# Kernel tuning notes

Hardware: AMD Instinct MI355X
Metric: run time of the kernel (lower is better)

Reference implementation:

```python
import jax, jax.numpy as jnp
import numpy as np

B, T, D, E, H = 4, 1024, 1024, 8, 2048


def setup_inputs() -> dict:
    key = jax.random.key(0)
    ks = jax.random.split(key, 5)
    # Kaiming-uniform-ish init scales (exact values irrelevant for correctness baseline)
    bound_bank = 1.0 / np.sqrt(D)
    bound_down = 1.0 / np.sqrt(H)
    return {
        "x": jax.random.normal(ks[0], (B, T, D), dtype=jnp.float32),
        "gate_w": jax.random.uniform(ks[1], (E, D), jnp.float32, -bound_bank, bound_bank),
        "gate_bank": jax.random.uniform(ks[2], (E, D, H), jnp.float32, -bound_bank, bound_bank),
        "up_bank": jax.random.uniform(ks[3], (E, D, H), jnp.float32, -bound_bank, bound_bank),
        "down_bank": jax.random.uniform(ks[4], (E, H, D), jnp.float32, -bound_down, bound_down),
    }


def reference(x, gate_w, gate_bank, up_bank, down_bank):
    # Router logits: [B,T,E] (nn.Linear with weight [E,D], no bias)
    logits = jnp.einsum('btd,ed->bte', x, gate_w)
    selected = jnp.argmax(logits, axis=-1)          # [B,T] int
    # Dense all-expert SwiGLU
    u = jnp.einsum('btd,edh->bteh', x, up_bank)     # [B,T,E,H]
    a = jnp.einsum('btd,edh->bteh', x, gate_bank)   # [B,T,E,H]
    h = jax.nn.silu(a) * u                          # [B,T,E,H]
    y = jnp.einsum('bteh,ehd->bted', h, down_bank)  # [B,T,E,D]
    # Gather argmax-selected expert output per token
    idx = selected[:, :, None, None]                # [B,T,1,1]
    out = jnp.take_along_axis(y, idx, axis=2)[:, :, 0, :]  # [B,T,D]
    return out
```

## Files before the change

### kernel.cpp

```cpp
#include <hip/hip_runtime.h>
#include <hip/hip_bf16.h>

#define NTOK 4096
#define DDIM 1024
#define HDIM 2048
#define NEXP 8

typedef __attribute__((ext_vector_type(4))) float f32x4;
typedef __attribute__((ext_vector_type(8))) short bf16x8;
typedef __attribute__((ext_vector_type(8))) unsigned short us8;

__device__ __forceinline__ unsigned short f2bf(float f) {
    unsigned u = __float_as_uint(f);
    return (unsigned short)((u + 0x7fffu + ((u >> 16) & 1u)) >> 16);
}

__device__ __forceinline__ void gload16(const void* g, void* l) {
    __builtin_amdgcn_global_load_lds((const __attribute__((address_space(1))) void*)g,
                                     (__attribute__((address_space(3))) void*)l, 16, 0, 0);
}

__global__ __launch_bounds__(256) void xg_kernel(
        const float* __restrict__ x, const float* __restrict__ gw,
        unsigned short* __restrict__ xb, int* __restrict__ sel) {
    const int t = blockIdx.x, tid = threadIdx.x, lane = tid & 63, w = tid >> 6;
    const float4 v = *reinterpret_cast<const float4*>(x + (size_t)t * DDIM + tid * 4);
    ushort4 o = { f2bf(v.x), f2bf(v.y), f2bf(v.z), f2bf(v.w) };
    *reinterpret_cast<ushort4*>(xb + (size_t)t * DDIM + tid * 4) = o;

    double acc[NEXP];
    #pragma unroll
    for (int e = 0; e < NEXP; ++e) {
        const float4 g = *reinterpret_cast<const float4*>(gw + (size_t)e * DDIM + tid * 4);
        acc[e] = (double)v.x * g.x + (double)v.y * g.y + (double)v.z * g.z + (double)v.w * g.w;
    }
    __shared__ double red[4][NEXP];
    #pragma unroll
    for (int e = 0; e < NEXP; ++e) {
        double a = acc[e];
        #pragma unroll
        for (int off = 32; off; off >>= 1) a += __shfl_down(a, off);
        if (lane == 0) red[w][e] = a;
    }
    __syncthreads();
    if (tid == 0) {
        int best = 0; double bv = -1e300;
        #pragma unroll
        for (int e = 0; e < NEXP; ++e) {
            double s = red[0][e] + red[1][e] + red[2][e] + red[3][e];
            if (s > bv) { bv = s; best = e; }
        }
        sel[t] = best;
    }
}

__global__ void scatter_kernel(const int* __restrict__ sel, int* __restrict__ cnt,
                               int* __restrict__ perm) {
    int t = blockIdx.x * blockDim.x + threadIdx.x;
    if (t < NTOK) {
        int e = sel[t];
        int p = atomicAdd(&cnt[e], 1);
        perm[e * NTOK + p] = t;
    }
}

__global__ __launch_bounds__(256) void tcast(const float* __restrict__ src,
        unsigned short* __restrict__ dst, int R, int C, int interleave, int upoff,
        long long estride) {
    __shared__ unsigned short tile[64][65];
    const int e = blockIdx.z, r0 = blockIdx.y * 64, c0 = blockIdx.x * 64;
    const float* s = src + ((size_t)e * R + r0) * C + c0;
    const int t = threadIdx.x;
    const int rd = t >> 2;
    #pragma unroll
    for (int j = 0; j < 4; ++j) {
        int c4 = (t & 3) * 4 + j;
        float4 v = *reinterpret_cast<const float4*>(s + (size_t)rd * C + c4 * 4);
        tile[c4 * 4 + 0][rd] = f2bf(v.x);
        tile[c4 * 4 + 1][rd] = f2bf(v.y);
        tile[c4 * 4 + 2][rd] = f2bf(v.z);
        tile[c4 * 4 + 3][rd] = f2bf(v.w);
    }
    __syncthreads();
    const int cr = t >> 2;
    const int c = c0 + cr;
    const int orow = interleave ? (((c >> 4) << 5) + (c & 15) + upoff) : c;
    unsigned short* drow = dst + (size_t)e * estride + (size_t)orow * R + r0;
    const int rbase = (t & 3) * 16;
    us8 v0, v1;
    #pragma unroll
    for (int s2 = 0; s2 < 8; ++s2) ((unsigned short*)&v0)[s2] = tile[cr][rbase + s2];
    #pragma unroll
    for (int s2 = 0; s2 < 8; ++s2) ((unsigned short*)&v1)[s2] = tile[cr][rbase + 8 + s2];
    *reinterpret_cast<us8*>(drow + rbase) = v0;
    *reinterpret_cast<us8*>(drow + rbase + 8) = v1;
}

__global__ __launch_bounds__(256) void stage_a(
        const unsigned short* __restrict__ xb, const unsigned short* __restrict__ wa,
        const int* __restrict__ cnt, const int* __restrict__ perm,
        unsigned short* __restrict__ hws) {
    const int e = blockIdx.z;
    const int n0 = blockIdx.x * 128;
    const int m0 = blockIdx.y * 128;
    const int count = cnt[e];
    if (m0 >= count) return;
    const int* pl = perm + e * NTOK;

    __shared__ unsigned short __attribute__((aligned(16))) As[2][128 * 64];
    __shared__ unsigned short __attribute__((aligned(16))) Bs[2][128 * 64];

    const int tid = threadIdx.x, lane = tid & 63, w = tid >> 6;
    const int wr = w >> 1, wc = w & 1, li = lane & 15, lg = lane >> 4;
    const int sb = lane & 7, r8 = lane >> 3;
    const int srcswz = (sb ^ r8) * 8;

    const unsigned short* pA[4];
    const unsigned short* pB[4];
    #pragma unroll
    for (int i = 0; i < 4; ++i) {
        int row = i * 32 + w * 8 + r8;
        int tr = m0 + row; if (tr >= count) tr = count - 1;
        int tok = pl[tr];
        pA[i] = xb + (size_t)tok * DDIM + srcswz;
        pB[i] = wa + ((size_t)e * (2 * HDIM) + (size_t)(n0 + row)) * DDIM + srcswz;
    }

    f32x4 acc[4][4];
    #pragma unroll
    for (int i = 0; i < 4; ++i)
        #pragma unroll
        for (int j = 0; j < 4; ++j) acc[i][j] = (f32x4){0.f, 0.f, 0.f, 0.f};

    #pragma unroll
    for (int i = 0; i < 4; ++i) gload16(pA[i], &As[0][(i * 256 + w * 64) * 8]);
    #pragma unroll
    for (int i = 0; i < 4; ++i) gload16(pB[i], &Bs[0][(i * 256 + w * 64) * 8]);
    asm volatile("s_waitcnt vmcnt(0)" ::: "memory");
    __syncthreads();

    int cur = 0;
    const int NT = DDIM / 64;
    for (int t = 0; t < NT; ++t) {
        if (t + 1 < NT) {
            const int k0 = (t + 1) * 64;
            #pragma unroll
            for (int i = 0; i < 4; ++i) gload16(pA[i] + k0, &As[cur ^ 1][(i * 256 + w * 64) * 8]);
            #pragma unroll
            for (int i = 0; i < 4; ++i) gload16(pB[i] + k0, &Bs[cur ^ 1][(i * 256 + w * 64) * 8]);
        }
        #pragma unroll
        for (int kf = 0; kf < 2; ++kf) {
            bf16x8 a[4], b[4];
            const int kb = kf * 4 + lg;
            #pragma unroll
            for (int mi = 0; mi < 4; ++mi) {
                int r = wr * 64 + mi * 16 + li;
                a[mi] = *reinterpret_cast<const bf16x8*>(&As[cur][r * 64 + ((kb ^ (li & 7)) << 3)]);
            }
            #pragma unroll
            for (int ni = 0; ni < 4; ++ni) {
                int n = wc * 64 + ni * 16 + li;
                b[ni] = *reinterpret_cast<const bf16x8*>(&Bs[cur][n * 64 + ((kb ^ (li & 7)) << 3)]);
            }
            #pragma unroll
            for (int mi = 0; mi < 4; ++mi)
                #pragma unroll
                for (int ni = 0; ni < 4; ++ni)
                    acc[mi][ni] = __builtin_amdgcn_mfma_f32_16x16x32_bf16(a[mi], b[ni], acc[mi][ni], 0, 0, 0);
        }
        if (t + 1 < NT) {
            asm volatile("s_waitcnt vmcnt(0)" ::: "memory");
            __syncthreads();
            cur ^= 1;
        }
    }
    const int hbase = (n0 >> 1) + wc * 32 + li;
    #pragma unroll
    for (int mi = 0; mi < 4; ++mi) {
        #pragma unroll
        for (int r = 0; r < 4; ++r) {
            int row = m0 + wr * 64 + mi * 16 + lg * 4 + r;
            if (row < count) {
                int tok = pl[row];
                #pragma unroll
                for (int p = 0; p < 2; ++p) {
                    float a = acc[mi][p * 2 + 0][r];
                    float u = acc[mi][p * 2 + 1][r];
                    float h = (a / (1.f + __expf(-a))) * u;
                    hws[(size_t)tok * HDIM + hbase + p * 16] = f2bf(h);
                }
            }
        }
    }
}

__global__ __launch_bounds__(256) void stage_b(
        const unsigned short* __restrict__ hws, const unsigned short* __restrict__ wb,
        const int* __restrict__ cnt, const int* __restrict__ perm,
        float* __restrict__ out) {
    const int e = blockIdx.z;
    const int n0 = blockIdx.x * 128;
    const int m0 = blockIdx.y * 128;
    const int count = cnt[e];
    if (m0 >= count) return;
    const int* pl = perm + e * NTOK;

    __shared__ unsigned short __attribute__((aligned(16))) As[2][128 * 64];
    __shared__ unsigned short __attribute__((aligned(16))) Bs[2][128 * 64];

    const int tid = threadIdx.x, lane = tid & 63, w = tid >> 6;
    const int wr = w >> 1, wc = w & 1, li = lane & 15, lg = lane >> 4;
    const int sb = lane & 7, r8 = lane >> 3;
    const int srcswz = (sb ^ r8) * 8;

    const unsigned short* pA[4];
    const unsigned short* pB[4];
    #pragma unroll
    for (int i = 0; i < 4; ++i) {
        int row = i * 32 + w * 8 + r8;
        int tr = m0 + row; if (tr >= count) tr = count - 1;
        int tok = pl[tr];
        pA[i] = hws + (size_t)tok * HDIM + srcswz;
        pB[i] = wb + ((size_t)e * DDIM + (size_t)(n0 + row)) * HDIM + srcswz;
    }

    f32x4 acc[4][4];
    #pragma unroll
    for (int i = 0; i < 4; ++i)
        #pragma unroll
        for (int j = 0; j < 4; ++j) acc[i][j] = (f32x4){0.f, 0.f, 0.f, 0.f};

    #pragma unroll
    for (int i = 0; i < 4; ++i) gload16(pA[i], &As[0][(i * 256 + w * 64) * 8]);
    #pragma unroll
    for (int i = 0; i < 4; ++i) gload16(pB[i], &Bs[0][(i * 256 + w * 64) * 8]);
    asm volatile("s_waitcnt vmcnt(0)" ::: "memory");
    __syncthreads();

    int cur = 0;
    const int NT = HDIM / 64;
    for (int t = 0; t < NT; ++t) {
        if (t + 1 < NT) {
            const int k0 = (t + 1) * 64;
            #pragma unroll
            for (int i = 0; i < 4; ++i) gload16(pA[i] + k0, &As[cur ^ 1][(i * 256 + w * 64) * 8]);
            #pragma unroll
            for (int i = 0; i < 4; ++i) gload16(pB[i] + k0, &Bs[cur ^ 1][(i * 256 + w * 64) * 8]);
        }
        #pragma unroll
        for (int kf = 0; kf < 2; ++kf) {
            bf16x8 a[4], b[4];
            const int kb = kf * 4 + lg;
            #pragma unroll
            for (int mi = 0; mi < 4; ++mi) {
                int r = wr * 64 + mi * 16 + li;
                a[mi] = *reinterpret_cast<const bf16x8*>(&As[cur][r * 64 + ((kb ^ (li & 7)) << 3)]);
            }
            #pragma unroll
            for (int ni = 0; ni < 4; ++ni) {
                int n = wc * 64 + ni * 16 + li;
                b[ni] = *reinterpret_cast<const bf16x8*>(&Bs[cur][n * 64 + ((kb ^ (li & 7)) << 3)]);
            }
            #pragma unroll
            for (int mi = 0; mi < 4; ++mi)
                #pragma unroll
                for (int ni = 0; ni < 4; ++ni)
                    acc[mi][ni] = __builtin_amdgcn_mfma_f32_16x16x32_bf16(a[mi], b[ni], acc[mi][ni], 0, 0, 0);
        }
        if (t + 1 < NT) {
            asm volatile("s_waitcnt vmcnt(0)" ::: "memory");
            __syncthreads();
            cur ^= 1;
        }
    }
    #pragma unroll
    for (int mi = 0; mi < 4; ++mi) {
        #pragma unroll
        for (int r = 0; r < 4; ++r) {
            int row = m0 + wr * 64 + mi * 16 + lg * 4 + r;
            if (row < count) {
                int tok = pl[row];
                #pragma unroll
                for (int ni = 0; ni < 4; ++ni)
                    out[(size_t)tok * DDIM + n0 + wc * 64 + ni * 16 + li] = acc[mi][ni][r];
            }
        }
    }
}

extern "C" void kernel_launch(void* const* d_in, const int* in_sizes, int n_in,
                              void* d_out, int out_size, void* d_ws, size_t ws_size,
                              hipStream_t stream) {
    const float* x  = (const float*)d_in[0];
    const float* gw = (const float*)d_in[1];
    const float* gb = (const float*)d_in[2];
    const float* ub = (const float*)d_in[3];
    const float* db = (const float*)d_in[4];
    float* out = (float*)d_out;

    char* ws = (char*)d_ws;
    unsigned short* wbank = (unsigned short*)(ws);
    unsigned short* hws   = (unsigned short*)(ws + 67108864);
    unsigned short* xbf   = (unsigned short*)(ws + 67108864 + 16777216);
    char* misc = ws + 67108864 + 16777216 + 8388608;
    int* cnt  = (int*)(misc);
    int* sel  = (int*)(misc + 256);
    int* perm = (int*)(misc + 256 + 16384);

    hipMemsetAsync(cnt, 0, 256, stream);
    xg_kernel<<<NTOK, 256, 0, stream>>>(x, gw, xbf, sel);
    tcast<<<dim3(HDIM / 64, DDIM / 64, NEXP), 256, 0, stream>>>(
        gb, wbank, DDIM, HDIM, 1, 0, (long long)2 * HDIM * DDIM);
    tcast<<<dim3(HDIM / 64, DDIM / 64, NEXP), 256, 0, stream>>>(
        ub, wbank, DDIM, HDIM, 1, 16, (long long)2 * HDIM * DDIM);
    scatter_kernel<<<NTOK / 256, 256, 0, stream>>>(sel, cnt, perm);
    stage_a<<<dim3(2 * HDIM / 128, NTOK / 128, NEXP), 256, 0, stream>>>(
        xbf, wbank, cnt, perm, hws);
    tcast<<<dim3(DDIM / 64, HDIM / 64, NEXP), 256, 0, stream>>>(
        db, wbank, HDIM, DDIM, 0, 0, (long long)DDIM * HDIM);
    stage_b<<<dim3(DDIM / 128, NTOK / 128, NEXP), 256, 0, stream>>>(
        hws, wbank, cnt, perm, out);
}
```

Measured before the change: 368.5 us.

## Pre-pack weights into MFMA fragment layout and load B directly from global

The weight cast kernel now writes bf16 weights in a fragment-major layout, with 512-element blocks per (16-column block, 32-k slice). This lets each lane fetch its MFMA B operand with one contiguous 16-byte global load. Both GEMM stages drop the B shared-memory buffer and its async staging, halving LDS use, and occupancy hints of 3 blocks per SM are added. In exchange, B reads are no longer shared through LDS between the two row-warps, so L2/global traffic rises, and the global load latency now sits directly in the MFMA loop with no prefetch.

```diff
diff --git a/kernel.cpp b/kernel.cpp
--- a/kernel.cpp
+++ b/kernel.cpp
@@ -64,10 +64,10 @@
     }
 }
 
-__global__ __launch_bounds__(256) void tcast(const float* __restrict__ src,
-        unsigned short* __restrict__ dst, int R, int C, int interleave, int upoff,
-        long long estride) {
-    __shared__ unsigned short tile[64][65];
+__global__ __launch_bounds__(256) void fcast(const float* __restrict__ src,
+        unsigned short* __restrict__ dst, int R, int C, int NB, int KS,
+        int interleave, int qsel, long long estride) {
+    __shared__ unsigned short tile[64][72];
     const int e = blockIdx.z, r0 = blockIdx.y * 64, c0 = blockIdx.x * 64;
     const float* s = src + ((size_t)e * R + r0) * C + c0;
     const int t = threadIdx.x;
@@ -82,33 +82,29 @@
         tile[c4 * 4 + 3][rd] = f2bf(v.w);
     }
     __syncthreads();
-    const int cr = t >> 2;
-    const int c = c0 + cr;
-    const int orow = interleave ? (((c >> 4) << 5) + (c & 15) + upoff) : c;
-    unsigned short* drow = dst + (size_t)e * estride + (size_t)orow * R + r0;
-    const int rbase = (t & 3) * 16;
-    us8 v0, v1;
-    #pragma unroll
-    for (int s2 = 0; s2 < 8; ++s2) ((unsigned short*)&v0)[s2] = tile[cr][rbase + s2];
-    #pragma unroll
-    for (int s2 = 0; s2 < 8; ++s2) ((unsigned short*)&v1)[s2] = tile[cr][rbase + 8 + s2];
-    *reinterpret_cast<us8*>(drow + rbase) = v0;
-    *reinterpret_cast<us8*>(drow + rbase + 8) = v1;
-}
-
-__global__ __launch_bounds__(256) void stage_a(
+    const int q = t >> 6, l = t & 63, li = l & 15, lg = l >> 4;
+    const int nblk = interleave ? (((c0 >> 4) + q) * 2 + qsel) : ((c0 >> 4) + q);
+    #pragma unroll
+    for (int kf2 = 0; kf2 < 2; ++kf2) {
+        const int ks = (r0 >> 5) + kf2;
+        us8 v = *reinterpret_cast<const us8*>(&tile[q * 16 + li][kf2 * 32 + lg * 8]);
+        *reinterpret_cast<us8*>(dst + ((size_t)e * estride) +
+            (((size_t)nblk * KS + ks) << 9) + l * 8) = v;
+    }
+}
+
+__global__ __launch_bounds__(256, 3) void stage_a(
         const unsigned short* __restrict__ xb, const unsigned short* __restrict__ wa,
         const int* __restrict__ cnt, const int* __restrict__ perm,
         unsigned short* __restrict__ hws) {
     const int e = blockIdx.z;
-    const int n0 = blockIdx.x * 128;
+    const int bx = blockIdx.x;
     const int m0 = blockIdx.y * 128;
     const int count = cnt[e];
     if (m0 >= count) return;
     const int* pl = perm + e * NTOK;
 
     __shared__ unsigned short __attribute__((aligned(16))) As[2][128 * 64];
-    __shared__ unsigned short __attribute__((aligned(16))) Bs[2][128 * 64];
 
     const int tid = threadIdx.x, lane = tid & 63, w = tid >> 6;
     const int wr = w >> 1, wc = w & 1, li = lane & 15, lg = lane >> 4;
@@ -116,15 +112,14 @@
     const int srcswz = (sb ^ r8) * 8;
 
     const unsigned short* pA[4];
-    const unsigned short* pB[4];
     #pragma unroll
     for (int i = 0; i < 4; ++i) {
         int row = i * 32 + w * 8 + r8;
         int tr = m0 + row; if (tr >= count) tr = count - 1;
-        int tok = pl[tr];
-        pA[i] = xb + (size_t)tok * DDIM + srcswz;
-        pB[i] = wa + ((size_t)e * (2 * HDIM) + (size_t)(n0 + row)) * DDIM + srcswz;
-    }
+        pA[i] = xb + (size_t)pl[tr] * DDIM + srcswz;
+    }
+    const unsigned short* bp = wa + (((size_t)e * 256 + bx * 8 + wc * 4) << 5 << 9)
+                               + (size_t)lane * 8;
 
     f32x4 acc[4][4];
     #pragma unroll
@@ -134,8 +129,6 @@
 
     #pragma unroll
     for (int i = 0; i < 4; ++i) gload16(pA[i], &As[0][(i * 256 + w * 64) * 8]);
-    #pragma unroll
-    for (int i = 0; i < 4; ++i) gload16(pB[i], &Bs[0][(i * 256 + w * 64) * 8]);
     asm volatile("s_waitcnt vmcnt(0)" ::: "memory");
     __syncthreads();
 
@@ -146,24 +139,20 @@
             const int k0 = (t + 1) * 64;
             #pragma unroll
             for (int i = 0; i < 4; ++i) gload16(pA[i] + k0, &As[cur ^ 1][(i * 256 + w * 64) * 8]);
-            #pragma unroll
-            for (int i = 0; i < 4; ++i) gload16(pB[i] + k0, &Bs[cur ^ 1][(i * 256 + w * 64) * 8]);
         }
         #pragma unroll
         for (int kf = 0; kf < 2; ++kf) {
+            const int kb = kf * 4 + lg;
             bf16x8 a[4], b[4];
-            const int kb = kf * 4 + lg;
+            #pragma unroll
+            for (int ni = 0; ni < 4; ++ni)
+                b[ni] = *reinterpret_cast<const bf16x8*>(bp + (((size_t)(ni * 32 + t * 2 + kf)) << 9));
             #pragma unroll
             for (int mi = 0; mi < 4; ++mi) {
                 int r = wr * 64 + mi * 16 + li;
                 a[mi] = *reinterpret_cast<const bf16x8*>(&As[cur][r * 64 + ((kb ^ (li & 7)) << 3)]);
             }
             #pragma unroll
-            for (int ni = 0; ni < 4; ++ni) {
-                int n = wc * 64 + ni * 16 + li;
-                b[ni] = *reinterpret_cast<const bf16x8*>(&Bs[cur][n * 64 + ((kb ^ (li & 7)) << 3)]);
-            }
-            #pragma unroll
             for (int mi = 0; mi < 4; ++mi)
                 #pragma unroll
                 for (int ni = 0; ni < 4; ++ni)
@@ -175,7 +164,7 @@
             cur ^= 1;
         }
     }
-    const int hbase = (n0 >> 1) + wc * 32 + li;
+    const int hbase = bx * 64 + wc * 32 + li;
     #pragma unroll
     for (int mi = 0; mi < 4; ++mi) {
         #pragma unroll
@@ -195,19 +184,18 @@
     }
 }
 
-__global__ __launch_bounds__(256) void stage_b(
+__global__ __launch_bounds__(256, 3) void stage_b(
         const unsigned short* __restrict__ hws, const unsigned short* __restrict__ wb,
         const int* __restrict__ cnt, const int* __restrict__ perm,
         float* __restrict__ out) {
     const int e = blockIdx.z;
-    const int n0 = blockIdx.x * 128;
+    const int bx = blockIdx.x;
     const int m0 = blockIdx.y * 128;
     const int count = cnt[e];
     if (m0 >= count) return;
     const int* pl = perm + e * NTOK;
 
     __shared__ unsigned short __attribute__((aligned(16))) As[2][128 * 64];
-    __shared__ unsigned short __attribute__((aligned(16))) Bs[2][128 * 64];
 
     const int tid = threadIdx.x, lane = tid & 63, w = tid >> 6;
     const int wr = w >> 1, wc = w & 1, li = lane & 15, lg = lane >> 4;
@@ -215,15 +203,14 @@
     const int srcswz = (sb ^ r8) * 8;
 
     const unsigned short* pA[4];
-    const unsigned short* pB[4];
     #pragma unroll
     for (int i = 0; i < 4; ++i) {
         int row = i * 32 + w * 8 + r8;
         int tr = m0 + row; if (tr >= count) tr = count - 1;
-        int tok = pl[tr];
-        pA[i] = hws + (size_t)tok * HDIM + srcswz;
-        pB[i] = wb + ((size_t)e * DDIM + (size_t)(n0 + row)) * HDIM + srcswz;
-    }
+        pA[i] = hws + (size_t)pl[tr] * HDIM + srcswz;
+    }
+    const unsigned short* bp = wb + (((size_t)e * 64 + bx * 8 + wc * 4) * 64 << 9)
+                               + (size_t)lane * 8;
 
     f32x4 acc[4][4];
     #pragma unroll
@@ -233,8 +220,6 @@
 
     #pragma unroll
     for (int i = 0; i < 4; ++i) gload16(pA[i], &As[0][(i * 256 + w * 64) * 8]);
-    #pragma unroll
-    for (int i = 0; i < 4; ++i) gload16(pB[i], &Bs[0][(i * 256 + w * 64) * 8]);
     asm volatile("s_waitcnt vmcnt(0)" ::: "memory");
     __syncthreads();
 
@@ -245,24 +230,20 @@
             const int k0 = (t + 1) * 64;
             #pragma unroll
             for (int i = 0; i < 4; ++i) gload16(pA[i] + k0, &As[cur ^ 1][(i * 256 + w * 64) * 8]);
-            #pragma unroll
-            for (int i = 0; i < 4; ++i) gload16(pB[i] + k0, &Bs[cur ^ 1][(i * 256 + w * 64) * 8]);
         }
         #pragma unroll
         for (int kf = 0; kf < 2; ++kf) {
+            const int kb = kf * 4 + lg;
             bf16x8 a[4], b[4];
-            const int kb = kf * 4 + lg;
+            #pragma unroll
+            for (int ni = 0; ni < 4; ++ni)
+                b[ni] = *reinterpret_cast<const bf16x8*>(bp + (((size_t)(ni * 64 + t * 2 + kf)) << 9));
             #pragma unroll
             for (int mi = 0; mi < 4; ++mi) {
                 int r = wr * 64 + mi * 16 + li;
                 a[mi] = *reinterpret_cast<const bf16x8*>(&As[cur][r * 64 + ((kb ^ (li & 7)) << 3)]);
             }
             #pragma unroll
-            for (int ni = 0; ni < 4; ++ni) {
-                int n = wc * 64 + ni * 16 + li;
-                b[ni] = *reinterpret_cast<const bf16x8*>(&Bs[cur][n * 64 + ((kb ^ (li & 7)) << 3)]);
-            }
-            #pragma unroll
             for (int mi = 0; mi < 4; ++mi)
                 #pragma unroll
                 for (int ni = 0; ni < 4; ++ni)
@@ -274,6 +255,7 @@
             cur ^= 1;
         }
     }
+    const int cbase = bx * 128 + wc * 64 + li;
     #pragma unroll
     for (int mi = 0; mi < 4; ++mi) {
         #pragma unroll
@@ -283,7 +265,7 @@
                 int tok = pl[row];
                 #pragma unroll
                 for (int ni = 0; ni < 4; ++ni)
-                    out[(size_t)tok * DDIM + n0 + wc * 64 + ni * 16 + li] = acc[mi][ni][r];
+                    out[(size_t)tok * DDIM + cbase + ni * 16] = acc[mi][ni][r];
             }
         }
     }
@@ -310,15 +292,15 @@
 
     hipMemsetAsync(cnt, 0, 256, stream);
     xg_kernel<<<NTOK, 256, 0, stream>>>(x, gw, xbf, sel);
-    tcast<<<dim3(HDIM / 64, DDIM / 64, NEXP), 256, 0, stream>>>(
-        gb, wbank, DDIM, HDIM, 1, 0, (long long)2 * HDIM * DDIM);
-    tcast<<<dim3(HDIM / 64, DDIM / 64, NEXP), 256, 0, stream>>>(
-        ub, wbank, DDIM, HDIM, 1, 16, (long long)2 * HDIM * DDIM);
+    fcast<<<dim3(HDIM / 64, DDIM / 64, NEXP), 256, 0, stream>>>(
+        gb, wbank, DDIM, HDIM, 256, 32, 1, 0, (long long)256 * 32 * 512);
+    fcast<<<dim3(HDIM / 64, DDIM / 64, NEXP), 256, 0, stream>>>(
+        ub, wbank, DDIM, HDIM, 256, 32, 1, 1, (long long)256 * 32 * 512);
     scatter_kernel<<<NTOK / 256, 256, 0, stream>>>(sel, cnt, perm);
     stage_a<<<dim3(2 * HDIM / 128, NTOK / 128, NEXP), 256, 0, stream>>>(
         xbf, wbank, cnt, perm, hws);
-    tcast<<<dim3(DDIM / 64, HDIM / 64, NEXP), 256, 0, stream>>>(
-        db, wbank, HDIM, DDIM, 0, 0, (long long)DDIM * HDIM);
+    fcast<<<dim3(DDIM / 64, HDIM / 64, NEXP), 256, 0, stream>>>(
+        db, wbank, HDIM, DDIM, 64, 64, 0, 0, (long long)64 * 64 * 512);
     stage_b<<<dim3(DDIM / 128, NTOK / 128, NEXP), 256, 0, stream>>>(
         hws, wbank, cnt, perm, out);
 }
```

New measurement: 382.4 us. 3.8% more time.
